# Kernel tuning notes

Measured on AMD Instinct MI355X. Metric: run time of the kernel, lower is better.

Reference implementation:

```python
import jax, jax.numpy as jnp
import numpy as np

D_MODEL = 1024
N_HEADS = 16
HEAD_DIM = D_MODEL // N_HEADS
SEQ_LEN = 2048
SPARSITY = 0.1


def make_local_mask(seq_len: int, sparsity: float) -> np.ndarray:
    # Replicates torch _generate_sparse_mask for pattern='local':
    # row i keeps columns j with i - w//2 <= j <= i + w//2, w = int(seq_len*sparsity)
    w = int(seq_len * sparsity)
    i = np.arange(seq_len)[:, None]
    j = np.arange(seq_len)[None, :]
    return (j >= i - w // 2) & (j <= i + w // 2)  # bool [S, S]


def setup_inputs() -> dict:
    key = jax.random.key(0)
    ks = jax.random.split(key, 9)
    s = 0.02
    inp = {
        "x": jax.random.normal(ks[0], (2, SEQ_LEN, D_MODEL), dtype=jnp.float32),
        "Wq": jax.random.normal(ks[1], (D_MODEL, D_MODEL), dtype=jnp.float32) * s,
        "bq": jnp.zeros((D_MODEL,), dtype=jnp.float32),
        "Wk": jax.random.normal(ks[2], (D_MODEL, D_MODEL), dtype=jnp.float32) * s,
        "bk": jnp.zeros((D_MODEL,), dtype=jnp.float32),
        "Wv": jax.random.normal(ks[3], (D_MODEL, D_MODEL), dtype=jnp.float32) * s,
        "bv": jnp.zeros((D_MODEL,), dtype=jnp.float32),
        "Wo": jax.random.normal(ks[4], (D_MODEL, D_MODEL), dtype=jnp.float32) * s,
        "bo": jnp.zeros((D_MODEL,), dtype=jnp.float32),
        "sparse_mask": jnp.asarray(make_local_mask(SEQ_LEN, SPARSITY)),
    }
    return inp


def reference(x, Wq, bq, Wk, bk, Wv, bv, Wo, bo, sparse_mask):
    B, S, D = x.shape
    H, Hd = N_HEADS, HEAD_DIM

    def proj(W, b):
        return (x @ W.T + b).reshape(B, S, H, Hd).transpose(0, 2, 1, 3)  # [B,H,S,Hd]

    Q = proj(Wq, bq)
    K = proj(Wk, bk)
    V = proj(Wv, bv)

    scores = jnp.einsum("bhqd,bhkd->bhqk", Q, K) / jnp.sqrt(jnp.float32(Hd))
    scores = jnp.where(sparse_mask[None, None, :S, :S], scores, -jnp.inf)
    attn = jax.nn.softmax(scores, axis=-1)  # [B,H,S,S]
    out = jnp.einsum("bhqk,bhkd->bhqd", attn, V)
    out = out.transpose(0, 2, 1, 3).reshape(B, S, D)
    return out @ Wo.T + bo
```

## Files before the change

### kernel.cpp

```cpp
#include <hip/hip_runtime.h>


#define SEQ    2048
#define DMODEL 1024
#define NHEAD  16
#define HDIM   64
#define HALFW  102
#define BWMAX  240
#define VTS    2176

typedef unsigned short u16;
typedef __attribute__((ext_vector_type(8))) short bf16x8;
typedef __attribute__((ext_vector_type(8))) _Float16 f16x8;
typedef __attribute__((ext_vector_type(4))) float f32x4;

#define VMW12() asm volatile("s_waitcnt vmcnt(12)" ::: "memory")
#define VMW10() asm volatile("s_waitcnt vmcnt(10)" ::: "memory")
#define VMW8()  asm volatile("s_waitcnt vmcnt(8)"  ::: "memory")
#define VMW5()  asm volatile("s_waitcnt vmcnt(5)"  ::: "memory")
#define VMW4()  asm volatile("s_waitcnt vmcnt(4)"  ::: "memory")
#define VMW0()  asm volatile("s_waitcnt vmcnt(0)"  ::: "memory")
#define BARR()  __builtin_amdgcn_s_barrier()
#define CFENCE() asm volatile("" ::: "memory")

__device__ __forceinline__ u16 f2bf(float f) {
    unsigned u = __builtin_bit_cast(unsigned, f);
    unsigned r = (u + 0x7fffu + ((u >> 16) & 1u)) >> 16;
    return (u16)r;
}
__device__ __forceinline__ float bf2f(u16 u) {
    return __builtin_bit_cast(float, ((unsigned)u) << 16);
}
__device__ __forceinline__ u16 f2h(float f) {
    return __builtin_bit_cast(u16, (_Float16)f);
}

__device__ __forceinline__ void gload16(const void* g, void* l) {
    __builtin_amdgcn_global_load_lds(
        (const __attribute__((address_space(1))) void*)g,
        (__attribute__((address_space(3))) void*)l, 16, 0, 0);
}

__global__ __launch_bounds__(256) void split5(
    const float* __restrict__ x,  const float* __restrict__ wq,
    const float* __restrict__ wk, const float* __restrict__ wv,
    const float* __restrict__ wo,
    u16* __restrict__ xh, u16* __restrict__ wbase)
{
    const int y = blockIdx.y;
    const float* src; u16* dst; int nblk;
    switch (y) {
      case 0:  src = x;  dst = xh;              nblk = 4096; break;
      case 1:  src = wq; dst = wbase;           nblk = 1024; break;
      case 2:  src = wk; dst = wbase + 1048576; nblk = 1024; break;
      case 3:  src = wv; dst = wbase + 2097152; nblk = 1024; break;
      default: src = wo; dst = wbase + 3145728; nblk = 1024; break;
    }
    const int bx = blockIdx.x;
    if (bx >= nblk) return;
    const int i = (bx * 256 + threadIdx.x) * 4;
    const float4 v = *(const float4*)(src + i);
    ushort4 h;
    h.x = f2h(v.x); h.y = f2h(v.y); h.z = f2h(v.z); h.w = f2h(v.w);
    *(ushort4*)(dst + i) = h;
}

__global__ __launch_bounds__(256) void gemm_qkvf(
    const u16* __restrict__ xh, const u16* __restrict__ wbase,
    const float* __restrict__ bq, const float* __restrict__ bk,
    const float* __restrict__ bvv,
    u16* __restrict__ Qo, u16* __restrict__ Ko, u16* __restrict__ VTo)
{
    __shared__ u16 sA[4][4096];
    __shared__ u16 sB[4][3][2048];

    const int tid = threadIdx.x, ln = tid & 63, wv = tid >> 6;
    const int wm = wv >> 1, wn = wv & 1;
    const int srow = ln & 15, scol = (ln >> 4) * 8;

    const int bx = blockIdx.x;
    const int mt = (bx & 7) * 4 + ((bx >> 3) & 3);
    const int nt = bx >> 5;
    const int m0 = mt * 128, n0 = nt * 64;

    f32x4 acc[3][4][2];
#pragma unroll
    for (int y = 0; y < 3; ++y)
#pragma unroll
        for (int fm = 0; fm < 4; ++fm)
#pragma unroll
            for (int fn = 0; fn < 2; ++fn) acc[y][fm][fn] = (f32x4){0.f, 0.f, 0.f, 0.f};

    auto stage = [&](int s) {
        const int buf = s & 3, k0 = s << 5;
#pragma unroll
        for (int i = 0; i < 2; ++i) {
            const int c = wv * 2 + i;
            gload16(xh + (size_t)(m0 + c * 16 + srow) * 1024 + k0 + scol,
                    sA[buf] + c * 512);
        }
#pragma unroll
        for (int i = 0; i < 3; ++i) {
            const int c = wv * 3 + i;
            const int yy = c >> 2, g = c & 3;
            gload16(wbase + (size_t)yy * 1048576
                          + (size_t)(n0 + g * 16 + srow) * 1024 + k0 + scol,
                    sB[buf][yy] + g * 512);
        }
    };

    stage(0); stage(1);

    for (int t = 0; t < 32; ++t) {
        if (t + 2 < 32) stage(t + 2);
        if (t < 30)       VMW10();
        else if (t == 30) VMW5();
        else              VMW0();
        BARR();
        CFENCE();

        const int buf = t & 3;
        f16x8 a[4];
#pragma unroll
        for (int f = 0; f < 4; ++f)
            a[f] = *(const f16x8*)(sA[buf] + (wm * 4 + f) * 512 + ln * 8);
#pragma unroll
        for (int y = 0; y < 3; ++y) {
            f16x8 b[2];
#pragma unroll
            for (int f = 0; f < 2; ++f)
                b[f] = *(const f16x8*)(sB[buf][y] + (wn * 2 + f) * 512 + ln * 8);
#pragma unroll
            for (int fm = 0; fm < 4; ++fm)
#pragma unroll
                for (int fn = 0; fn < 2; ++fn)
                    acc[y][fm][fn] = __builtin_amdgcn_mfma_f32_16x16x32_f16(
                        a[fm], b[fn], acc[y][fm][fn], 0, 0, 0);
        }
    }

    const int rl = ln & 15, kh = ln >> 4;

#pragma unroll
    for (int y = 0; y < 2; ++y) {
        const float* bias = y ? bk : bq;
        u16* Y = y ? Ko : Qo;
#pragma unroll
        for (int fn = 0; fn < 2; ++fn) {
            const int n = n0 + wn * 32 + fn * 16 + rl;
            const float bb = bias[n];
            const int h = n >> 6, hd = n & 63;
#pragma unroll
            for (int fm = 0; fm < 4; ++fm)
#pragma unroll
                for (int r = 0; r < 4; ++r) {
                    const int m = m0 + wm * 64 + fm * 16 + kh * 4 + r;
                    const int b = m >> 11, s = m & (SEQ - 1);
                    Y[((size_t)(b * NHEAD + h) * SEQ + s) * HDIM + hd] =
                        f2bf(acc[y][fm][fn][r] + bb);
                }
        }
    }
#pragma unroll
    for (int fn = 0; fn < 2; ++fn) {
        const int n = n0 + wn * 32 + fn * 16 + rl;
        const float bb = bvv[n];
        const int h = n >> 6, hd = n & 63;
#pragma unroll
        for (int fm = 0; fm < 4; ++fm)
#pragma unroll
            for (int r = 0; r < 4; ++r) {
                const int m = m0 + wm * 64 + fm * 16 + kh * 4 + r;
                const int b = m >> 11, s = m & (SEQ - 1);
                VTo[((size_t)(b * NHEAD + h) * HDIM + hd) * VTS + s] =
                    f2bf(acc[2][fm][fn][r] + bb);
            }
    }
}

__device__ __forceinline__ void gemm_core_out(
    const u16* __restrict__ A, const u16* __restrict__ B,
    int m0, int n0, u16 (*sA)[4096], u16 (*sB)[4096], f32x4 acc[4][4])
{
    const int tid = threadIdx.x, ln = tid & 63, wave = tid >> 6;
    const int wm = wave >> 1, wn = wave & 1;
    const int srow = ln & 15, scol = (ln >> 4) * 8;

#pragma unroll
    for (int fm = 0; fm < 4; ++fm)
#pragma unroll
        for (int fn = 0; fn < 4; ++fn) acc[fm][fn] = (f32x4){0.f, 0.f, 0.f, 0.f};

    auto stage = [&](int s) {
        if (s >= 32) return;
        const int buf = s % 5;
        const int k0 = s << 5;
#pragma unroll
        for (int c = wave; c < 8; c += 4) {
            gload16(A + (size_t)(m0 + c * 16 + srow) * 1024 + k0 + scol, sA[buf] + c * 512);
            gload16(B + (size_t)(n0 + c * 16 + srow) * 1024 + k0 + scol, sB[buf] + c * 512);
        }
    };

    stage(0); stage(1); stage(2);

    int buf = 0;
    for (int t = 0; t < 32; ++t) {
        stage(t + 3);
        if (t < 29)       VMW12();
        else if (t == 29) VMW8();
        else if (t == 30) VMW4();
        else              VMW0();
        BARR();
        CFENCE();

        f16x8 a[4], b[4];
#pragma unroll
        for (int f = 0; f < 4; ++f) {
            a[f] = *(const f16x8*)(sA[buf] + (wm * 4 + f) * 512 + ln * 8);
            b[f] = *(const f16x8*)(sB[buf] + (wn * 4 + f) * 512 + ln * 8);
        }
#pragma unroll
        for (int fm = 0; fm < 4; ++fm)
#pragma unroll
            for (int fn = 0; fn < 4; ++fn)
                acc[fm][fn] = __builtin_amdgcn_mfma_f32_16x16x32_f16(
                    a[fm], b[fn], acc[fm][fn], 0, 0, 0);
        buf = (buf == 4) ? 0 : buf + 1;
    }
}

__global__ __launch_bounds__(256) void gemm_out(
    const u16* __restrict__ A, const u16* __restrict__ B,
    const float* __restrict__ bias, float* __restrict__ Y)
{
    __shared__ u16 sA[5][4096], sB[5][4096];
    const int bx = blockIdx.x;
    const int mt = (bx & 7) * 4 + (bx >> 6);
    const int nt = (bx >> 3) & 7;
    const int m0 = mt * 128, n0 = nt * 128;

    f32x4 acc[4][4];
    gemm_core_out(A, B, m0, n0, sA, sB, acc);

    const int tid = threadIdx.x, ln = tid & 63, wave = tid >> 6;
    const int wm = wave >> 1, wn = wave & 1;
    const int rl = ln & 15, kh = ln >> 4;
#pragma unroll
    for (int fn = 0; fn < 4; ++fn) {
        const int n = n0 + wn * 64 + fn * 16 + rl;
        const float bb = bias[n];
#pragma unroll
        for (int fm = 0; fm < 4; ++fm)
#pragma unroll
            for (int r = 0; r < 4; ++r) {
                const int m = m0 + wm * 64 + fm * 16 + kh * 4 + r;
                Y[(size_t)m * DMODEL + n] = acc[fm][fn][r] + bb;
            }
    }
}

__global__ __launch_bounds__(256) void attn_mfma(
    const u16* __restrict__ Q, const u16* __restrict__ K,
    const u16* __restrict__ VT, u16* __restrict__ aoh)
{
    __shared__ u16 P_lds[4][16][232];

    const int tid = threadIdx.x, ln = tid & 63, wv = tid >> 6;
    const int bx0 = blockIdx.x;
    const int asg = (bx0 & 7) * 128 + (bx0 >> 3);
    const int bh  = asg >> 5;
    const int qt  = asg & 31;
    const int b   = bh >> 4, h = bh & 15;
    const int q0  = qt * 64 + wv * 16;
    const int jmin = (q0 >= 104) ? (q0 - 104) : 0;

    const u16* Qbh  = Q  + (size_t)bh * SEQ * HDIM;
    const u16* Kbh  = K  + (size_t)bh * SEQ * HDIM;
    const u16* VTbh = VT + (size_t)bh * HDIM * VTS;

    const int lr = ln & 15, lk = ln >> 4;

    const bf16x8 qf0 = *(const bf16x8*)(Qbh + (size_t)(q0 + lr) * HDIM + lk * 8);
    const bf16x8 qf1 = *(const bf16x8*)(Qbh + (size_t)(q0 + lr) * HDIM + 32 + lk * 8);

    f32x4 sc[14];
#pragma unroll
    for (int t = 0; t < 14; ++t) {
        const int j  = jmin + t * 16 + lr;
        const int jc = min(j, SEQ - 1);
        const u16* kp = Kbh + (size_t)jc * HDIM + lk * 8;
        const bf16x8 k0 = *(const bf16x8*)kp;
        const bf16x8 k1 = *(const bf16x8*)(kp + 32);
        f32x4 a = (f32x4){0.f, 0.f, 0.f, 0.f};
        a = __builtin_amdgcn_mfma_f32_16x16x32_bf16(qf0, k0, a, 0, 0, 0);
        a = __builtin_amdgcn_mfma_f32_16x16x32_bf16(qf1, k1, a, 0, 0, 0);
        sc[t] = a;
    }

    float lrow[4];
#pragma unroll
    for (int r = 0; r < 4; ++r) {
        const int i = q0 + lk * 4 + r;
        float mx = -3.0e38f;
#pragma unroll
        for (int t = 0; t < 14; ++t) {
            const int j = jmin + t * 16 + lr;
            float v = sc[t][r] * 0.125f;
            const bool ok = (j >= i - HALFW) && (j <= i + HALFW) && (j < SEQ);
            v = ok ? v : -3.0e38f;
            sc[t][r] = v;
            mx = fmaxf(mx, v);
        }
#pragma unroll
        for (int off = 8; off > 0; off >>= 1) mx = fmaxf(mx, __shfl_xor(mx, off));
        float sum = 0.f;
#pragma unroll
        for (int t = 0; t < 14; ++t) {
            const float p = __expf(sc[t][r] - mx);
            sum += p;
            P_lds[wv][lk * 4 + r][t * 16 + lr] = f2bf(p);
        }
#pragma unroll
        for (int off = 8; off > 0; off >>= 1) sum += __shfl_xor(sum, off);
        lrow[r] = sum;
    }

    f32x4 ao[4];
#pragma unroll
    for (int nt = 0; nt < 4; ++nt) ao[nt] = (f32x4){0.f, 0.f, 0.f, 0.f};
#pragma unroll
    for (int kc = 0; kc < 7; ++kc) {
        const bf16x8 pf = *(const bf16x8*)&P_lds[wv][lr][kc * 32 + lk * 8];
        const int jb = jmin + kc * 32 + lk * 8;
#pragma unroll
        for (int nt = 0; nt < 4; ++nt) {
            const bf16x8 vf = *(const bf16x8*)(VTbh + (size_t)(nt * 16 + lr) * VTS + jb);
            ao[nt] = __builtin_amdgcn_mfma_f32_16x16x32_bf16(pf, vf, ao[nt], 0, 0, 0);
        }
    }

#pragma unroll
    for (int nt = 0; nt < 4; ++nt)
#pragma unroll
        for (int r = 0; r < 4; ++r) {
            const int i = q0 + lk * 4 + r;
            const float o = ao[nt][r] / lrow[r];
            aoh[((size_t)b * SEQ + i) * DMODEL + h * HDIM + nt * 16 + lr] = f2h(o);
        }
}

template<int QKV>
__global__ __launch_bounds__(256) void gemm_xwt(
    const float* __restrict__ X, const float* __restrict__ W,
    const float* __restrict__ bias, float* __restrict__ Y)
{
    __shared__ float As[16][132];
    __shared__ float Bs[16][68];
    const int tid = threadIdx.x;
    const int bx  = blockIdx.x;
    const int n0  = (bx & 15) * 64;
    const int m0  = (bx >> 4) * 128;
    const int ty  = tid >> 4, tx = tid & 15;
    float acc[8][4];
#pragma unroll
    for (int r = 0; r < 8; ++r)
#pragma unroll
        for (int c = 0; c < 4; ++c) acc[r][c] = 0.f;
    const int lrow = tid >> 2, lkq = (tid & 3) * 4;
    for (int k0 = 0; k0 < DMODEL; k0 += 16) {
        float4 a0 = *(const float4*)(X + (size_t)(m0 + lrow)      * DMODEL + k0 + lkq);
        float4 a1 = *(const float4*)(X + (size_t)(m0 + lrow + 64) * DMODEL + k0 + lkq);
        float4 b0 = *(const float4*)(W + (size_t)(n0 + lrow)      * DMODEL + k0 + lkq);
        __syncthreads();
        As[lkq + 0][lrow] = a0.x; As[lkq + 1][lrow] = a0.y;
        As[lkq + 2][lrow] = a0.z; As[lkq + 3][lrow] = a0.w;
        As[lkq + 0][lrow + 64] = a1.x; As[lkq + 1][lrow + 64] = a1.y;
        As[lkq + 2][lrow + 64] = a1.z; As[lkq + 3][lrow + 64] = a1.w;
        Bs[lkq + 0][lrow] = b0.x; Bs[lkq + 1][lrow] = b0.y;
        Bs[lkq + 2][lrow] = b0.z; Bs[lkq + 3][lrow] = b0.w;
        __syncthreads();
#pragma unroll
        for (int k = 0; k < 16; ++k) {
            float4 av0 = *(const float4*)&As[k][ty * 8];
            float4 av1 = *(const float4*)&As[k][ty * 8 + 4];
            float4 bv  = *(const float4*)&Bs[k][tx * 4];
            float a[8] = {av0.x, av0.y, av0.z, av0.w, av1.x, av1.y, av1.z, av1.w};
            float bb[4] = {bv.x, bv.y, bv.z, bv.w};
#pragma unroll
            for (int r = 0; r < 8; ++r)
#pragma unroll
                for (int c = 0; c < 4; ++c) acc[r][c] += a[r] * bb[c];
        }
    }
    const float4 bb = *(const float4*)(bias + n0 + tx * 4);
    if (QKV) {
        const int b = m0 >> 11, h = n0 >> 6;
#pragma unroll
        for (int r = 0; r < 8; ++r) {
            const int m = m0 + ty * 8 + r, ss = m & (SEQ - 1);
            float4 o = {acc[r][0] + bb.x, acc[r][1] + bb.y, acc[r][2] + bb.z, acc[r][3] + bb.w};
            *(float4*)(Y + ((size_t)(b * NHEAD + h) * SEQ + ss) * HDIM + tx * 4) = o;
        }
    } else {
#pragma unroll
        for (int r = 0; r < 8; ++r) {
            const int m = m0 + ty * 8 + r;
            float4 o = {acc[r][0] + bb.x, acc[r][1] + bb.y, acc[r][2] + bb.z, acc[r][3] + bb.w};
            *(float4*)(Y + (size_t)m * DMODEL + n0 + tx * 4) = o;
        }
    }
}

__global__ __launch_bounds__(256) void attn_local_f32(
    const float* __restrict__ Q, const float* __restrict__ K,
    const float* __restrict__ V, float* __restrict__ O)
{
    __shared__ float ssc[32][BWMAX];
    const int tid = threadIdx.x;
    const int bx0 = blockIdx.x;
    const int bx  = (bx0 & 7) * 256 + (bx0 >> 3);
    const int qt  = bx & 63;
    const int h   = (bx >> 6) & 15;
    const int b   = bx >> 10;
    const int i0  = qt * 32;
    const int jmin = max(0, i0 - HALFW);
    const int jmax = min(SEQ - 1, i0 + 31 + HALFW);
    const int BWt  = jmax - jmin + 1;
    const float* Qbh = Q + (size_t)(b * NHEAD + h) * SEQ * HDIM;
    const float* Kbh = K + (size_t)(b * NHEAD + h) * SEQ * HDIM;
    const float* Vbh = V + (size_t)(b * NHEAD + h) * SEQ * HDIM;
    const int jj = tid;
    if (jj < BWt) {
        float acc[32];
#pragma unroll
        for (int i = 0; i < 32; ++i) acc[i] = 0.f;
        const float* kp = Kbh + (size_t)(jmin + jj) * HDIM;
        for (int d0 = 0; d0 < HDIM; d0 += 4) {
            const float4 kv = *(const float4*)(kp + d0);
#pragma unroll
            for (int i = 0; i < 32; ++i) {
                const float4 qv = *(const float4*)(Qbh + (size_t)(i0 + i) * HDIM + d0);
                acc[i] += qv.x * kv.x + qv.y * kv.y + qv.z * kv.z + qv.w * kv.w;
            }
        }
#pragma unroll
        for (int i = 0; i < 32; ++i) ssc[i][jj] = acc[i] * 0.125f;
    }
    __syncthreads();
    const int wv = tid >> 6, ln = tid & 63;
    float rs[8];
#pragma unroll
    for (int r = 0; r < 8; ++r) {
        const int i  = wv * 8 + r;
        const int qi = i0 + i;
        const int lo = max(0, qi - HALFW) - jmin;
        const int hi = min(SEQ - 1, qi + HALFW) - jmin;
        float m = -1e30f;
#pragma unroll
        for (int c = 0; c < 4; ++c) {
            const int j = ln + 64 * c;
            if (j >= lo && j <= hi) m = fmaxf(m, ssc[i][j]);
        }
#pragma unroll
        for (int off = 32; off > 0; off >>= 1) m = fmaxf(m, __shfl_xor(m, off));
        float sum = 0.f;
#pragma unroll
        for (int c = 0; c < 4; ++c) {
            const int j = ln + 64 * c;
            if (j < BWt) {
                float p = 0.f;
                if (j >= lo && j <= hi) p = __expf(ssc[i][j] - m);
                ssc[i][j] = p;
                sum += p;
            }
        }
#pragma unroll
        for (int off = 32; off > 0; off >>= 1) sum += __shfl_xor(sum, off);
        rs[r] = sum;
    }
    float oa[8];
#pragma unroll
    for (int r = 0; r < 8; ++r) oa[r] = 0.f;
    int jq = 0;
    for (; jq + 4 <= BWt; jq += 4) {
        const float v0 = Vbh[(size_t)(jmin + jq + 0) * HDIM + ln];
        const float v1 = Vbh[(size_t)(jmin + jq + 1) * HDIM + ln];
        const float v2 = Vbh[(size_t)(jmin + jq + 2) * HDIM + ln];
        const float v3 = Vbh[(size_t)(jmin + jq + 3) * HDIM + ln];
#pragma unroll
        for (int r = 0; r < 8; ++r) {
            const float4 p4 = *(const float4*)&ssc[wv * 8 + r][jq];
            oa[r] += p4.x * v0 + p4.y * v1 + p4.z * v2 + p4.w * v3;
        }
    }
    for (; jq < BWt; ++jq) {
        const float v0 = Vbh[(size_t)(jmin + jq) * HDIM + ln];
#pragma unroll
        for (int r = 0; r < 8; ++r) oa[r] += ssc[wv * 8 + r][jq] * v0;
    }
#pragma unroll
    for (int r = 0; r < 8; ++r) {
        const int i = i0 + wv * 8 + r;
        O[((size_t)b * SEQ + i) * DMODEL + h * HDIM + ln] = oa[r] / rs[r];
    }
}

extern "C" void kernel_launch(void* const* d_in, const int* in_sizes, int n_in,
                              void* d_out, int out_size, void* d_ws, size_t ws_size,
                              hipStream_t stream) {
    const float* x  = (const float*)d_in[0];
    const float* Wq = (const float*)d_in[1];
    const float* bq = (const float*)d_in[2];
    const float* Wk = (const float*)d_in[3];
    const float* bk = (const float*)d_in[4];
    const float* Wv = (const float*)d_in[5];
    const float* bv = (const float*)d_in[6];
    const float* Wo = (const float*)d_in[7];
    const float* bo = (const float*)d_in[8];

    float* out = (float*)d_out;

    const size_t REQUIRED = (size_t)80 * 1024 * 1024;
    if (ws_size >= REQUIRED) {
        const size_t M4 = 4194304;
        const size_t VT_ELEMS = (size_t)32 * HDIM * VTS;
        u16* Qb    = (u16*)d_ws;
        u16* Kb    = Qb + M4;
        u16* VTb   = Kb + M4;
        u16* aoh   = VTb + VT_ELEMS;
        u16* xh    = aoh + M4;
        u16* wbase = xh + M4;

        hipMemsetAsync(VTb, 0, VT_ELEMS * sizeof(u16), stream);
        split5<<<dim3(4096, 5), 256, 0, stream>>>(x, Wq, Wk, Wv, Wo, xh, wbase);
        gemm_qkvf<<<512, 256, 0, stream>>>(xh, wbase, bq, bk, bv, Qb, Kb, VTb);
        attn_mfma<<<1024, 256, 0, stream>>>(Qb, Kb, VTb, aoh);
        gemm_out<<<256, 256, 0, stream>>>(aoh, wbase + 3145728, bo, out);
    } else {
        float* ws = (float*)d_ws;
        const size_t NELEM = (size_t)2 * SEQ * DMODEL;
        float* Qb = ws;
        float* Kb = ws + NELEM;
        float* Vb = ws + 2 * NELEM;
        float* AO = ws + 3 * NELEM;
        gemm_xwt<1><<<512, 256, 0, stream>>>(x, Wq, bq, Qb);
        gemm_xwt<1><<<512, 256, 0, stream>>>(x, Wk, bk, Kb);
        gemm_xwt<1><<<512, 256, 0, stream>>>(x, Wv, bv, Vb);
        attn_local_f32<<<2048, 256, 0, stream>>>(Qb, Kb, Vb, AO);
        gemm_xwt<0><<<512, 256, 0, stream>>>(AO, Wo, bo, out);
    }
}
```

Measured before the change: 117.3 us.

## Convert QKV and output GEMMs to single-wave blocks without barriers

Both projection GEMMs move from 256-thread blocks with four cooperating waves to 64-thread single-wave blocks. Each wave stages its own smaller tile through LDS and waits only on its own vmcnt, so the per-iteration s_barrier goes away. The QKV GEMM also gains a third prefetch stage. The intent is to cut barrier stalls and raise the block count for better CU occupancy. The cost is that each wave now loads its whole A/B tile alone, with no reuse across waves, so global and LDS traffic per FLOP rises.

```diff
diff --git a/kernel.cpp b/kernel.cpp
--- a/kernel.cpp
+++ b/kernel.cpp
@@ -14,13 +14,13 @@
 typedef __attribute__((ext_vector_type(8))) _Float16 f16x8;
 typedef __attribute__((ext_vector_type(4))) float f32x4;
 
-#define VMW12() asm volatile("s_waitcnt vmcnt(12)" ::: "memory")
+#define VMW30() asm volatile("s_waitcnt vmcnt(30)" ::: "memory")
+#define VMW24() asm volatile("s_waitcnt vmcnt(24)" ::: "memory")
+#define VMW20() asm volatile("s_waitcnt vmcnt(20)" ::: "memory")
+#define VMW16() asm volatile("s_waitcnt vmcnt(16)" ::: "memory")
 #define VMW10() asm volatile("s_waitcnt vmcnt(10)" ::: "memory")
 #define VMW8()  asm volatile("s_waitcnt vmcnt(8)"  ::: "memory")
-#define VMW5()  asm volatile("s_waitcnt vmcnt(5)"  ::: "memory")
-#define VMW4()  asm volatile("s_waitcnt vmcnt(4)"  ::: "memory")
 #define VMW0()  asm volatile("s_waitcnt vmcnt(0)"  ::: "memory")
-#define BARR()  __builtin_amdgcn_s_barrier()
 #define CFENCE() asm volatile("" ::: "memory")
 
 __device__ __forceinline__ u16 f2bf(float f) {
@@ -65,23 +65,22 @@
     *(ushort4*)(dst + i) = h;
 }
 
-__global__ __launch_bounds__(256) void gemm_qkvf(
+__global__ __launch_bounds__(64) void gemm_qkvf_wave(
     const u16* __restrict__ xh, const u16* __restrict__ wbase,
     const float* __restrict__ bq, const float* __restrict__ bk,
     const float* __restrict__ bvv,
     u16* __restrict__ Qo, u16* __restrict__ Ko, u16* __restrict__ VTo)
 {
-    __shared__ u16 sA[4][4096];
-    __shared__ u16 sB[4][3][2048];
-
-    const int tid = threadIdx.x, ln = tid & 63, wv = tid >> 6;
-    const int wm = wv >> 1, wn = wv & 1;
+    __shared__ u16 sA[4][2048];
+    __shared__ u16 sB[4][3][1024];
+
+    const int ln = threadIdx.x & 63;
     const int srow = ln & 15, scol = (ln >> 4) * 8;
 
     const int bx = blockIdx.x;
-    const int mt = (bx & 7) * 4 + ((bx >> 3) & 3);
-    const int nt = bx >> 5;
-    const int m0 = mt * 128, n0 = nt * 64;
+    const int mt = (bx & 7) * 8 + ((bx >> 3) & 7);
+    const int nt = bx >> 6;
+    const int m0 = mt * 64, n0 = nt * 32;
 
     f32x4 acc[3][4][2];
 #pragma unroll
@@ -94,42 +93,39 @@
     auto stage = [&](int s) {
         const int buf = s & 3, k0 = s << 5;
 #pragma unroll
-        for (int i = 0; i < 2; ++i) {
-            const int c = wv * 2 + i;
+        for (int c = 0; c < 4; ++c)
             gload16(xh + (size_t)(m0 + c * 16 + srow) * 1024 + k0 + scol,
                     sA[buf] + c * 512);
-        }
-#pragma unroll
-        for (int i = 0; i < 3; ++i) {
-            const int c = wv * 3 + i;
-            const int yy = c >> 2, g = c & 3;
-            gload16(wbase + (size_t)yy * 1048576
-                          + (size_t)(n0 + g * 16 + srow) * 1024 + k0 + scol,
-                    sB[buf][yy] + g * 512);
-        }
+#pragma unroll
+        for (int y = 0; y < 3; ++y)
+#pragma unroll
+            for (int g = 0; g < 2; ++g)
+                gload16(wbase + (size_t)y * 1048576
+                              + (size_t)(n0 + g * 16 + srow) * 1024 + k0 + scol,
+                        sB[buf][y] + g * 512);
     };
 
-    stage(0); stage(1);
+    stage(0); stage(1); stage(2);
 
     for (int t = 0; t < 32; ++t) {
-        if (t + 2 < 32) stage(t + 2);
-        if (t < 30)       VMW10();
-        else if (t == 30) VMW5();
+        if (t + 3 < 32) stage(t + 3);
+        if (t < 29)       VMW30();
+        else if (t == 29) VMW20();
+        else if (t == 30) VMW10();
         else              VMW0();
-        BARR();
         CFENCE();
 
         const int buf = t & 3;
         f16x8 a[4];
 #pragma unroll
         for (int f = 0; f < 4; ++f)
-            a[f] = *(const f16x8*)(sA[buf] + (wm * 4 + f) * 512 + ln * 8);
+            a[f] = *(const f16x8*)(sA[buf] + f * 512 + ln * 8);
 #pragma unroll
         for (int y = 0; y < 3; ++y) {
             f16x8 b[2];
 #pragma unroll
             for (int f = 0; f < 2; ++f)
-                b[f] = *(const f16x8*)(sB[buf][y] + (wn * 2 + f) * 512 + ln * 8);
+                b[f] = *(const f16x8*)(sB[buf][y] + f * 512 + ln * 8);
 #pragma unroll
             for (int fm = 0; fm < 4; ++fm)
 #pragma unroll
@@ -147,14 +143,14 @@
         u16* Y = y ? Ko : Qo;
 #pragma unroll
         for (int fn = 0; fn < 2; ++fn) {
-            const int n = n0 + wn * 32 + fn * 16 + rl;
+            const int n = n0 + fn * 16 + rl;
             const float bb = bias[n];
             const int h = n >> 6, hd = n & 63;
 #pragma unroll
             for (int fm = 0; fm < 4; ++fm)
 #pragma unroll
                 for (int r = 0; r < 4; ++r) {
-                    const int m = m0 + wm * 64 + fm * 16 + kh * 4 + r;
+                    const int m = m0 + fm * 16 + kh * 4 + r;
                     const int b = m >> 11, s = m & (SEQ - 1);
                     Y[((size_t)(b * NHEAD + h) * SEQ + s) * HDIM + hd] =
                         f2bf(acc[y][fm][fn][r] + bb);
@@ -163,14 +159,14 @@
     }
 #pragma unroll
     for (int fn = 0; fn < 2; ++fn) {
-        const int n = n0 + wn * 32 + fn * 16 + rl;
+        const int n = n0 + fn * 16 + rl;
         const float bb = bvv[n];
         const int h = n >> 6, hd = n & 63;
 #pragma unroll
         for (int fm = 0; fm < 4; ++fm)
 #pragma unroll
             for (int r = 0; r < 4; ++r) {
-                const int m = m0 + wm * 64 + fm * 16 + kh * 4 + r;
+                const int m = m0 + fm * 16 + kh * 4 + r;
                 const int b = m >> 11, s = m & (SEQ - 1);
                 VTo[((size_t)(b * NHEAD + h) * HDIM + hd) * VTS + s] =
                     f2bf(acc[2][fm][fn][r] + bb);
@@ -178,25 +174,30 @@
     }
 }
 
-__device__ __forceinline__ void gemm_core_out(
+__global__ __launch_bounds__(64) void gemm_out_wave(
     const u16* __restrict__ A, const u16* __restrict__ B,
-    int m0, int n0, u16 (*sA)[4096], u16 (*sB)[4096], f32x4 acc[4][4])
+    const float* __restrict__ bias, float* __restrict__ Y)
 {
-    const int tid = threadIdx.x, ln = tid & 63, wave = tid >> 6;
-    const int wm = wave >> 1, wn = wave & 1;
+    __shared__ u16 sA[4][2048], sB[4][2048];
+
+    const int ln = threadIdx.x & 63;
     const int srow = ln & 15, scol = (ln >> 4) * 8;
 
+    const int bx = blockIdx.x;
+    const int mt = (bx & 7) * 8 + ((bx >> 3) & 7);
+    const int nt = bx >> 6;
+    const int m0 = mt * 64, n0 = nt * 64;
+
+    f32x4 acc[4][4];
 #pragma unroll
     for (int fm = 0; fm < 4; ++fm)
 #pragma unroll
         for (int fn = 0; fn < 4; ++fn) acc[fm][fn] = (f32x4){0.f, 0.f, 0.f, 0.f};
 
     auto stage = [&](int s) {
-        if (s >= 32) return;
-        const int buf = s % 5;
-        const int k0 = s << 5;
-#pragma unroll
-        for (int c = wave; c < 8; c += 4) {
+        const int buf = s & 3, k0 = s << 5;
+#pragma unroll
+        for (int c = 0; c < 4; ++c) {
             gload16(A + (size_t)(m0 + c * 16 + srow) * 1024 + k0 + scol, sA[buf] + c * 512);
             gload16(B + (size_t)(n0 + c * 16 + srow) * 1024 + k0 + scol, sB[buf] + c * 512);
         }
@@ -204,21 +205,20 @@
 
     stage(0); stage(1); stage(2);
 
-    int buf = 0;
     for (int t = 0; t < 32; ++t) {
-        stage(t + 3);
-        if (t < 29)       VMW12();
-        else if (t == 29) VMW8();
-        else if (t == 30) VMW4();
+        if (t + 3 < 32) stage(t + 3);
+        if (t < 29)       VMW24();
+        else if (t == 29) VMW16();
+        else if (t == 30) VMW8();
         else              VMW0();
-        BARR();
         CFENCE();
 
+        const int buf = t & 3;
         f16x8 a[4], b[4];
 #pragma unroll
         for (int f = 0; f < 4; ++f) {
-            a[f] = *(const f16x8*)(sA[buf] + (wm * 4 + f) * 512 + ln * 8);
-            b[f] = *(const f16x8*)(sB[buf] + (wn * 4 + f) * 512 + ln * 8);
+            a[f] = *(const f16x8*)(sA[buf] + f * 512 + ln * 8);
+            b[f] = *(const f16x8*)(sB[buf] + f * 512 + ln * 8);
         }
 #pragma unroll
         for (int fm = 0; fm < 4; ++fm)
@@ -226,35 +226,18 @@
             for (int fn = 0; fn < 4; ++fn)
                 acc[fm][fn] = __builtin_amdgcn_mfma_f32_16x16x32_f16(
                     a[fm], b[fn], acc[fm][fn], 0, 0, 0);
-        buf = (buf == 4) ? 0 : buf + 1;
-    }
-}
-
-__global__ __launch_bounds__(256) void gemm_out(
-    const u16* __restrict__ A, const u16* __restrict__ B,
-    const float* __restrict__ bias, float* __restrict__ Y)
-{
-    __shared__ u16 sA[5][4096], sB[5][4096];
-    const int bx = blockIdx.x;
-    const int mt = (bx & 7) * 4 + (bx >> 6);
-    const int nt = (bx >> 3) & 7;
-    const int m0 = mt * 128, n0 = nt * 128;
-
-    f32x4 acc[4][4];
-    gemm_core_out(A, B, m0, n0, sA, sB, acc);
-
-    const int tid = threadIdx.x, ln = tid & 63, wave = tid >> 6;
-    const int wm = wave >> 1, wn = wave & 1;
+    }
+
     const int rl = ln & 15, kh = ln >> 4;
 #pragma unroll
     for (int fn = 0; fn < 4; ++fn) {
-        const int n = n0 + wn * 64 + fn * 16 + rl;
+        const int n = n0 + fn * 16 + rl;
         const float bb = bias[n];
 #pragma unroll
         for (int fm = 0; fm < 4; ++fm)
 #pragma unroll
             for (int r = 0; r < 4; ++r) {
-                const int m = m0 + wm * 64 + fm * 16 + kh * 4 + r;
+                const int m = m0 + fm * 16 + kh * 4 + r;
                 Y[(size_t)m * DMODEL + n] = acc[fm][fn][r] + bb;
             }
     }
@@ -534,9 +517,9 @@
 
         hipMemsetAsync(VTb, 0, VT_ELEMS * sizeof(u16), stream);
         split5<<<dim3(4096, 5), 256, 0, stream>>>(x, Wq, Wk, Wv, Wo, xh, wbase);
-        gemm_qkvf<<<512, 256, 0, stream>>>(xh, wbase, bq, bk, bv, Qb, Kb, VTb);
+        gemm_qkvf_wave<<<2048, 64, 0, stream>>>(xh, wbase, bq, bk, bv, Qb, Kb, VTb);
         attn_mfma<<<1024, 256, 0, stream>>>(Qb, Kb, VTb, aoh);
-        gemm_out<<<256, 256, 0, stream>>>(aoh, wbase + 3145728, bo, out);
+        gemm_out_wave<<<1024, 64, 0, stream>>>(aoh, wbase + 3145728, bo, out);
     } else {
         float* ws = (float*)d_ws;
         const size_t NELEM = (size_t)2 * SEQ * DMODEL;
```

Result: slower. 165.7 us (+41.3%).

## Halve output GEMM tile width to 512 blocks and compact conversion grid

Applied to the files above, without the earlier changes.

The output projection GEMM now uses 128x64 tiles, launching 512 blocks instead of 256 so more CUs are occupied on a GPU with many compute units. Its pipeline shrinks from a 5-buffer, 3-ahead prefetch to a 4-buffer, 2-ahead prefetch with adjusted vmcnt waits, and each wave issues three loads per stage. The fp32-to-fp16 conversion kernel switches from a 2D grid where many blocks exited early to a dense 1D grid of 8192 blocks. Narrower tiles mean more A reloads and a shallower prefetch depth, which may expose more memory latency.

```diff
diff --git a/kernel.cpp b/kernel.cpp
--- a/kernel.cpp
+++ b/kernel.cpp
@@ -14,11 +14,10 @@
 typedef __attribute__((ext_vector_type(8))) _Float16 f16x8;
 typedef __attribute__((ext_vector_type(4))) float f32x4;
 
-#define VMW12() asm volatile("s_waitcnt vmcnt(12)" ::: "memory")
 #define VMW10() asm volatile("s_waitcnt vmcnt(10)" ::: "memory")
-#define VMW8()  asm volatile("s_waitcnt vmcnt(8)"  ::: "memory")
+#define VMW6()  asm volatile("s_waitcnt vmcnt(6)"  ::: "memory")
 #define VMW5()  asm volatile("s_waitcnt vmcnt(5)"  ::: "memory")
-#define VMW4()  asm volatile("s_waitcnt vmcnt(4)"  ::: "memory")
+#define VMW3()  asm volatile("s_waitcnt vmcnt(3)"  ::: "memory")
 #define VMW0()  asm volatile("s_waitcnt vmcnt(0)"  ::: "memory")
 #define BARR()  __builtin_amdgcn_s_barrier()
 #define CFENCE() asm volatile("" ::: "memory")
@@ -47,18 +46,21 @@
     const float* __restrict__ wo,
     u16* __restrict__ xh, u16* __restrict__ wbase)
 {
-    const int y = blockIdx.y;
-    const float* src; u16* dst; int nblk;
-    switch (y) {
-      case 0:  src = x;  dst = xh;              nblk = 4096; break;
-      case 1:  src = wq; dst = wbase;           nblk = 1024; break;
-      case 2:  src = wk; dst = wbase + 1048576; nblk = 1024; break;
-      case 3:  src = wv; dst = wbase + 2097152; nblk = 1024; break;
-      default: src = wo; dst = wbase + 3145728; nblk = 1024; break;
-    }
     const int bx = blockIdx.x;
-    if (bx >= nblk) return;
-    const int i = (bx * 256 + threadIdx.x) * 4;
+    const float* src; u16* dst; int blk;
+    if (bx < 4096) {
+        src = x; dst = xh; blk = bx;
+    } else {
+        const int w = (bx - 4096) >> 10;
+        blk = (bx - 4096) & 1023;
+        switch (w) {
+          case 0:  src = wq; dst = wbase;           break;
+          case 1:  src = wk; dst = wbase + 1048576; break;
+          case 2:  src = wv; dst = wbase + 2097152; break;
+          default: src = wo; dst = wbase + 3145728; break;
+        }
+    }
+    const int i = (blk * 256 + threadIdx.x) * 4;
     const float4 v = *(const float4*)(src + i);
     ushort4 h;
     h.x = f2h(v.x); h.y = f2h(v.y); h.z = f2h(v.z); h.w = f2h(v.w);
@@ -178,77 +180,71 @@
     }
 }
 
-__device__ __forceinline__ void gemm_core_out(
-    const u16* __restrict__ A, const u16* __restrict__ B,
-    int m0, int n0, u16 (*sA)[4096], u16 (*sB)[4096], f32x4 acc[4][4])
-{
-    const int tid = threadIdx.x, ln = tid & 63, wave = tid >> 6;
-    const int wm = wave >> 1, wn = wave & 1;
-    const int srow = ln & 15, scol = (ln >> 4) * 8;
-
-#pragma unroll
-    for (int fm = 0; fm < 4; ++fm)
-#pragma unroll
-        for (int fn = 0; fn < 4; ++fn) acc[fm][fn] = (f32x4){0.f, 0.f, 0.f, 0.f};
-
-    auto stage = [&](int s) {
-        if (s >= 32) return;
-        const int buf = s % 5;
-        const int k0 = s << 5;
-#pragma unroll
-        for (int c = wave; c < 8; c += 4) {
-            gload16(A + (size_t)(m0 + c * 16 + srow) * 1024 + k0 + scol, sA[buf] + c * 512);
-            gload16(B + (size_t)(n0 + c * 16 + srow) * 1024 + k0 + scol, sB[buf] + c * 512);
-        }
-    };
-
-    stage(0); stage(1); stage(2);
-
-    int buf = 0;
-    for (int t = 0; t < 32; ++t) {
-        stage(t + 3);
-        if (t < 29)       VMW12();
-        else if (t == 29) VMW8();
-        else if (t == 30) VMW4();
-        else              VMW0();
-        BARR();
-        CFENCE();
-
-        f16x8 a[4], b[4];
-#pragma unroll
-        for (int f = 0; f < 4; ++f) {
-            a[f] = *(const f16x8*)(sA[buf] + (wm * 4 + f) * 512 + ln * 8);
-            b[f] = *(const f16x8*)(sB[buf] + (wn * 4 + f) * 512 + ln * 8);
-        }
-#pragma unroll
-        for (int fm = 0; fm < 4; ++fm)
-#pragma unroll
-            for (int fn = 0; fn < 4; ++fn)
-                acc[fm][fn] = __builtin_amdgcn_mfma_f32_16x16x32_f16(
-                    a[fm], b[fn], acc[fm][fn], 0, 0, 0);
-        buf = (buf == 4) ? 0 : buf + 1;
-    }
-}
-
 __global__ __launch_bounds__(256) void gemm_out(
     const u16* __restrict__ A, const u16* __restrict__ B,
     const float* __restrict__ bias, float* __restrict__ Y)
 {
-    __shared__ u16 sA[5][4096], sB[5][4096];
+    __shared__ u16 sA[4][4096], sB[4][2048];
+
+    const int tid = threadIdx.x, ln = tid & 63, wv = tid >> 6;
+    const int wm = wv >> 1, wn = wv & 1;
+    const int srow = ln & 15, scol = (ln >> 4) * 8;
+
     const int bx = blockIdx.x;
-    const int mt = (bx & 7) * 4 + (bx >> 6);
-    const int nt = (bx >> 3) & 7;
-    const int m0 = mt * 128, n0 = nt * 128;
-
-    f32x4 acc[4][4];
-    gemm_core_out(A, B, m0, n0, sA, sB, acc);
-
-    const int tid = threadIdx.x, ln = tid & 63, wave = tid >> 6;
-    const int wm = wave >> 1, wn = wave & 1;
+    const int mt = (bx & 7) * 4 + ((bx >> 3) & 3);
+    const int nt = bx >> 5;
+    const int m0 = mt * 128, n0 = nt * 64;
+
+    f32x4 acc[4][2];
+#pragma unroll
+    for (int fm = 0; fm < 4; ++fm)
+#pragma unroll
+        for (int fn = 0; fn < 2; ++fn) acc[fm][fn] = (f32x4){0.f, 0.f, 0.f, 0.f};
+
+    auto stage = [&](int s) {
+        const int buf = s & 3, k0 = s << 5;
+#pragma unroll
+        for (int i = 0; i < 3; ++i) {
+            const int c = wv * 3 + i;
+            if (c < 8)
+                gload16(A + (size_t)(m0 + c * 16 + srow) * 1024 + k0 + scol,
+                        sA[buf] + c * 512);
+            else
+                gload16(B + (size_t)(n0 + (c - 8) * 16 + srow) * 1024 + k0 + scol,
+                        sB[buf] + (c - 8) * 512);
+        }
+    };
+
+    stage(0); stage(1);
+
+    for (int t = 0; t < 32; ++t) {
+        if (t + 2 < 32) stage(t + 2);
+        if (t < 30)       VMW6();
+        else if (t == 30) VMW3();
+        else              VMW0();
+        BARR();
+        CFENCE();
+
+        const int buf = t & 3;
+        f16x8 a[4], b[2];
+#pragma unroll
+        for (int f = 0; f < 4; ++f)
+            a[f] = *(const f16x8*)(sA[buf] + (wm * 4 + f) * 512 + ln * 8);
+#pragma unroll
+        for (int f = 0; f < 2; ++f)
+            b[f] = *(const f16x8*)(sB[buf] + (wn * 2 + f) * 512 + ln * 8);
+#pragma unroll
+        for (int fm = 0; fm < 4; ++fm)
+#pragma unroll
+            for (int fn = 0; fn < 2; ++fn)
+                acc[fm][fn] = __builtin_amdgcn_mfma_f32_16x16x32_f16(
+                    a[fm], b[fn], acc[fm][fn], 0, 0, 0);
+    }
+
     const int rl = ln & 15, kh = ln >> 4;
 #pragma unroll
-    for (int fn = 0; fn < 4; ++fn) {
-        const int n = n0 + wn * 64 + fn * 16 + rl;
+    for (int fn = 0; fn < 2; ++fn) {
+        const int n = n0 + wn * 32 + fn * 16 + rl;
         const float bb = bias[n];
 #pragma unroll
         for (int fm = 0; fm < 4; ++fm)
@@ -533,10 +529,10 @@
         u16* wbase = xh + M4;
 
         hipMemsetAsync(VTb, 0, VT_ELEMS * sizeof(u16), stream);
-        split5<<<dim3(4096, 5), 256, 0, stream>>>(x, Wq, Wk, Wv, Wo, xh, wbase);
+        split5<<<8192, 256, 0, stream>>>(x, Wq, Wk, Wv, Wo, xh, wbase);
         gemm_qkvf<<<512, 256, 0, stream>>>(xh, wbase, bq, bk, bv, Qb, Kb, VTb);
         attn_mfma<<<1024, 256, 0, stream>>>(Qb, Kb, VTb, aoh);
-        gemm_out<<<256, 256, 0, stream>>>(aoh, wbase + 3145728, bo, out);
+        gemm_out<<<512, 256, 0, stream>>>(aoh, wbase + 3145728, bo, out);
     } else {
         float* ws = (float*)d_ws;
         const size_t NELEM = (size_t)2 * SEQ * DMODEL;
```

After: 121.5 us. 1.04x slower.

## Stage shared K window in LDS for attention and flatten conversion grid

Applied to the files above, without the earlier changes.

The attention kernel now loads the union of K rows needed by all four waves of a block into swizzled LDS once, using direct global-to-LDS loads. Each wave then reads its K fragments from LDS instead of issuing redundant global loads, and the same buffer is reused for the P tile after a barrier. The fp32-to-half conversion kernel switches from a 2D grid with many idle early-exit blocks to a flat 1D grid with no wasted blocks. The cost is extra barriers, plus the risk of LDS bank conflicts if the swizzle and the later P reuse do not line up.

```diff
diff --git a/kernel.cpp b/kernel.cpp
--- a/kernel.cpp
+++ b/kernel.cpp
@@ -47,18 +47,21 @@
     const float* __restrict__ wo,
     u16* __restrict__ xh, u16* __restrict__ wbase)
 {
-    const int y = blockIdx.y;
-    const float* src; u16* dst; int nblk;
-    switch (y) {
-      case 0:  src = x;  dst = xh;              nblk = 4096; break;
-      case 1:  src = wq; dst = wbase;           nblk = 1024; break;
-      case 2:  src = wk; dst = wbase + 1048576; nblk = 1024; break;
-      case 3:  src = wv; dst = wbase + 2097152; nblk = 1024; break;
-      default: src = wo; dst = wbase + 3145728; nblk = 1024; break;
-    }
     const int bx = blockIdx.x;
-    if (bx >= nblk) return;
-    const int i = (bx * 256 + threadIdx.x) * 4;
+    const float* src; u16* dst; int blk;
+    if (bx < 4096) {
+        src = x; dst = xh; blk = bx;
+    } else {
+        const int w = (bx - 4096) >> 10;
+        blk = (bx - 4096) & 1023;
+        switch (w) {
+          case 0:  src = wq; dst = wbase;           break;
+          case 1:  src = wk; dst = wbase + 1048576; break;
+          case 2:  src = wv; dst = wbase + 2097152; break;
+          default: src = wo; dst = wbase + 3145728; break;
+        }
+    }
+    const int i = (blk * 256 + threadIdx.x) * 4;
     const float4 v = *(const float4*)(src + i);
     ushort4 h;
     h.x = f2h(v.x); h.y = f2h(v.y); h.z = f2h(v.z); h.w = f2h(v.w);
@@ -264,7 +267,7 @@
     const u16* __restrict__ Q, const u16* __restrict__ K,
     const u16* __restrict__ VT, u16* __restrict__ aoh)
 {
-    __shared__ u16 P_lds[4][16][232];
+    __shared__ u16 KP[17408];
 
     const int tid = threadIdx.x, ln = tid & 63, wv = tid >> 6;
     const int bx0 = blockIdx.x;
@@ -274,6 +277,8 @@
     const int b   = bh >> 4, h = bh & 15;
     const int q0  = qt * 64 + wv * 16;
     const int jmin = (q0 >= 104) ? (q0 - 104) : 0;
+    const int j0   = (qt * 64 >= 104) ? (qt * 64 - 104) : 0;
+    const int woff = jmin - j0;
 
     const u16* Qbh  = Q  + (size_t)bh * SEQ * HDIM;
     const u16* Kbh  = K  + (size_t)bh * SEQ * HDIM;
@@ -281,23 +286,38 @@
 
     const int lr = ln & 15, lk = ln >> 4;
 
+    {
+        const int sr = ln >> 3;
+        const int scol = ((ln & 7) ^ sr) * 8;
+        for (int c = wv; c < 34; c += 4) {
+            const int j = j0 + c * 8 + sr;
+            const int jc = (j < SEQ) ? j : (SEQ - 1);
+            gload16(Kbh + (size_t)jc * HDIM + scol, KP + c * 512);
+        }
+    }
+
     const bf16x8 qf0 = *(const bf16x8*)(Qbh + (size_t)(q0 + lr) * HDIM + lk * 8);
     const bf16x8 qf1 = *(const bf16x8*)(Qbh + (size_t)(q0 + lr) * HDIM + 32 + lk * 8);
 
+    __syncthreads();
+
     f32x4 sc[14];
 #pragma unroll
     for (int t = 0; t < 14; ++t) {
-        const int j  = jmin + t * 16 + lr;
-        const int jc = min(j, SEQ - 1);
-        const u16* kp = Kbh + (size_t)jc * HDIM + lk * 8;
-        const bf16x8 k0 = *(const bf16x8*)kp;
-        const bf16x8 k1 = *(const bf16x8*)(kp + 32);
+        const int row = woff + t * 16 + lr;
+        const int s0 = lk ^ (row & 7);
+        const int s1 = (4 + lk) ^ (row & 7);
+        const bf16x8 k0 = *(const bf16x8*)(KP + row * 64 + s0 * 8);
+        const bf16x8 k1 = *(const bf16x8*)(KP + row * 64 + s1 * 8);
         f32x4 a = (f32x4){0.f, 0.f, 0.f, 0.f};
         a = __builtin_amdgcn_mfma_f32_16x16x32_bf16(qf0, k0, a, 0, 0, 0);
         a = __builtin_amdgcn_mfma_f32_16x16x32_bf16(qf1, k1, a, 0, 0, 0);
         sc[t] = a;
     }
 
+    __syncthreads();
+
+    u16* P = KP + wv * 3712;
     float lrow[4];
 #pragma unroll
     for (int r = 0; r < 4; ++r) {
@@ -319,7 +339,7 @@
         for (int t = 0; t < 14; ++t) {
             const float p = __expf(sc[t][r] - mx);
             sum += p;
-            P_lds[wv][lk * 4 + r][t * 16 + lr] = f2bf(p);
+            P[(lk * 4 + r) * 232 + t * 16 + lr] = f2bf(p);
         }
 #pragma unroll
         for (int off = 8; off > 0; off >>= 1) sum += __shfl_xor(sum, off);
@@ -331,7 +351,7 @@
     for (int nt = 0; nt < 4; ++nt) ao[nt] = (f32x4){0.f, 0.f, 0.f, 0.f};
 #pragma unroll
     for (int kc = 0; kc < 7; ++kc) {
-        const bf16x8 pf = *(const bf16x8*)&P_lds[wv][lr][kc * 32 + lk * 8];
+        const bf16x8 pf = *(const bf16x8*)(P + lr * 232 + kc * 32 + lk * 8);
         const int jb = jmin + kc * 32 + lk * 8;
 #pragma unroll
         for (int nt = 0; nt < 4; ++nt) {
@@ -533,7 +553,7 @@
         u16* wbase = xh + M4;
 
         hipMemsetAsync(VTb, 0, VT_ELEMS * sizeof(u16), stream);
-        split5<<<dim3(4096, 5), 256, 0, stream>>>(x, Wq, Wk, Wv, Wo, xh, wbase);
+        split5<<<8192, 256, 0, stream>>>(x, Wq, Wk, Wv, Wo, xh, wbase);
         gemm_qkvf<<<512, 256, 0, stream>>>(xh, wbase, bq, bk, bv, Qb, Kb, VTb);
         attn_mfma<<<1024, 256, 0, stream>>>(Qb, Kb, VTb, aoh);
         gemm_out<<<256, 256, 0, stream>>>(aoh, wbase + 3145728, bo, out);
```

Result: faster. 105.9 us (-9.7%).
